# Kernel tuning notes

Hardware: AMD Instinct MI355X
Metric: run time of the kernel (lower is better)

Reference implementation:

```python
import jax, jax.numpy as jnp
import numpy as np

EPS = 1e-15
ATANH_CLIP = 1.0 - 1e-5
C = 1.0  # ball.c = |k|, k = -1.0
SQC = 1.0  # sqrt(C)


def _artanh(x):
    return jnp.arctanh(jnp.clip(x, -ATANH_CLIP, ATANH_CLIP))


def _norm(x):
    return jnp.linalg.norm(x, axis=-1, keepdims=True)


def mobius_add(x, y):
    x2 = jnp.sum(x * x, axis=-1, keepdims=True)
    y2 = jnp.sum(y * y, axis=-1, keepdims=True)
    xy = jnp.sum(x * y, axis=-1, keepdims=True)
    num = (1.0 + 2.0 * C * xy + C * y2) * x + (1.0 - C * x2) * y
    den = 1.0 + 2.0 * C * xy + (C ** 2) * x2 * y2
    return num / jnp.maximum(den, EPS)


def mobius_matvec(M, x):
    # x: [..., d_in], M: [d_out, d_in]
    x_norm = jnp.maximum(_norm(x), EPS)
    mx = x @ M.T
    mx_norm_raw = _norm(mx)
    mx_norm = jnp.maximum(mx_norm_raw, EPS)
    res = jnp.tanh(mx_norm / x_norm * _artanh(SQC * x_norm)) * mx / (mx_norm * SQC)
    return jnp.where(mx_norm_raw <= EPS, 0.0, res)


def mobius_pointwise_mul(w, x):
    x_norm = jnp.maximum(_norm(x), EPS)
    wx = w * x
    wx_norm_raw = _norm(wx)
    wx_norm = jnp.maximum(wx_norm_raw, EPS)
    res = jnp.tanh(wx_norm / x_norm * _artanh(SQC * x_norm)) * wx / (wx_norm * SQC)
    return jnp.where(wx_norm_raw <= EPS, 0.0, res)


def expmap0(u):
    un = jnp.maximum(_norm(u), EPS)
    return jnp.tanh(SQC * un) * u / (SQC * un)


def logmap0(y):
    yn = jnp.maximum(_norm(y), EPS)
    return _artanh(SQC * yn) * y / (SQC * yn)


def one_rnn_transform(W, h, U, x, b):
    Wh = mobius_matvec(W, h)
    Ux = mobius_matvec(U, x)
    return mobius_add(mobius_add(Wh, Ux), b)


def gru_cell(x, hx, weight_ih, weight_hh, bias):
    W_ir, W_ih, W_iz = jnp.split(weight_ih, 3, axis=0)
    W_hr, W_hh, W_hz = jnp.split(weight_hh, 3, axis=0)
    b_r, b_h, b_z = bias[0], bias[1], bias[2]
    z_t = jax.nn.sigmoid(logmap0(one_rnn_transform(W_hz, hx, W_iz, x, b_z)))
    r_t = jax.nn.sigmoid(logmap0(one_rnn_transform(W_hr, hx, W_ir, x, b_r)))
    rh_t = mobius_pointwise_mul(r_t, hx)
    h_tilde = one_rnn_transform(W_hh, rh_t, W_ih, x, b_h)
    delta_h = mobius_add(-hx, h_tilde)
    return mobius_add(hx, mobius_pointwise_mul(z_t, delta_h))


def gru_layer(x_seq, h0, weight_ih, weight_hh, bias):
    def step(hx, xt):
        h = gru_cell(xt, hx, weight_ih, weight_hh, bias)
        return h, h
    h_last, outs = jax.lax.scan(step, h0, x_seq)
    return outs, h_last


def setup_inputs() -> dict:
    key = jax.random.key(0)
    ks = jax.random.split(key, 8)
    T, B, D, H = 256, 64, 512, 512
    stdv = 1.0 / np.sqrt(H)
    inp = {
        # hyperbolic_input=True -> points must lie inside the unit ball; scale small
        "input": jax.random.normal(ks[0], (T, B, D), jnp.float32) * 0.01,
        "h0": jnp.zeros((2, B, H), jnp.float32),
        "weight_ih_1": jax.random.uniform(ks[1], (3 * H, D), jnp.float32, -stdv, stdv),
        "weight_ih_2": jax.random.uniform(ks[2], (3 * H, H), jnp.float32, -stdv, stdv),
        "weight_hh_1": jax.random.uniform(ks[3], (3 * H, H), jnp.float32, -stdv, stdv),
        "weight_hh_2": jax.random.uniform(ks[4], (3 * H, H), jnp.float32, -stdv, stdv),
        # biases initialized as expmap0(randn * 1e-5)
        "bias_1": expmap0(jax.random.normal(ks[5], (3, H), jnp.float32) * 1e-5),
        "bias_2": expmap0(jax.random.normal(ks[6], (3, H), jnp.float32) * 1e-5),
    }
    return inp


def reference(input, h0, weight_ih_1, weight_ih_2, weight_hh_1, weight_hh_2, bias_1, bias_2):
    # hyperbolic_input=True and hyperbolic_hidden_state0=True -> no initial expmap0
    out1, h_last1 = gru_layer(input, h0[0], weight_ih_1, weight_hh_1, bias_1)
    out2, h_last2 = gru_layer(out1, h0[1], weight_ih_2, weight_hh_2, bias_2)
    ht = jnp.stack([h_last1, h_last2])
    return out2, ht
```

## Files before the change

kernel.cpp:

```cpp
#include <hip/hip_runtime.h>
#include <hip/hip_fp16.h>
#include <math.h>
#include <stdint.h>


#define T_  256
#define B_  64
#define H_  512
#define G3_ 1536
#define EPSF 1e-15f
#define CLIPF (1.0f - 1e-5f)
#define SCOPE_AGENT __HIP_MEMORY_SCOPE_AGENT

typedef _Float16 v2h __attribute__((ext_vector_type(2)));

__device__ __forceinline__ float fdot2_(unsigned int w, unsigned int h, float c){
#if __has_builtin(__builtin_amdgcn_fdot2)
  return __builtin_amdgcn_fdot2(__builtin_bit_cast(v2h, w), __builtin_bit_cast(v2h, h), c, false);
#else
  const __half2 wh = __builtin_bit_cast(__half2, w);
  const __half2 hh = __builtin_bit_cast(__half2, h);
  return c + __low2float(wh)*__low2float(hh) + __high2float(wh)*__high2float(hh);
#endif
}

__device__ __forceinline__ float artanh_c(float x){
  x = fminf(fmaxf(x, -CLIPF), CLIPF);
  return 0.5f * logf((1.0f + x) / (1.0f - x));
}
__device__ __forceinline__ float sigmoidf_(float x){ return 1.0f/(1.0f+expf(-x)); }
__device__ __forceinline__ float hsum4(float4 v){ return (v.x+v.y)+(v.z+v.w); }

__device__ __forceinline__ void postf(unsigned long long* p, float x, unsigned tag){
  unsigned long long v = ((unsigned long long)tag << 32) |
                         (unsigned long long)__float_as_uint(x);
  __hip_atomic_store(p, v, __ATOMIC_RELAXED, SCOPE_AGENT);
}
__device__ __forceinline__ float pollf(const unsigned long long* p, unsigned tag){
  unsigned long long v = __hip_atomic_load(p, __ATOMIC_RELAXED, SCOPE_AGENT);
  while ((unsigned)(v >> 32) != tag)
    v = __hip_atomic_load(p, __ATOMIC_RELAXED, SCOPE_AGENT);
  return __uint_as_float((unsigned)v);
}

template<int NS>
__device__ __forceinline__ void wave_reduce_store(float (&v)[NS], float* red, int tid){
  #pragma unroll
  for (int off = 32; off > 0; off >>= 1)
    #pragma unroll
    for (int s = 0; s < NS; s++) v[s] += __shfl_xor(v[s], off);
  if ((tid & 63) == 0)
    #pragma unroll
    for (int s = 0; s < NS; s++) red[s*8 + (tid >> 6)] = v[s];
}

__global__ void k_prep_ih(const float* __restrict__ Wih, float* __restrict__ WihT){
  int i = blockIdx.x * blockDim.x + threadIdx.x;
  if (i >= H_ * G3_) return;
  int k = i / G3_, n = i % G3_;
  WihT[i] = Wih[n * H_ + k];
}

__device__ __forceinline__ uint4 pack8h(const float* s){
  __half2 p0 = __halves2half2(__float2half_rn(s[0]), __float2half_rn(s[1]));
  __half2 p1 = __halves2half2(__float2half_rn(s[2]), __float2half_rn(s[3]));
  __half2 p2 = __halves2half2(__float2half_rn(s[4]), __float2half_rn(s[5]));
  __half2 p3 = __halves2half2(__float2half_rn(s[6]), __float2half_rn(s[7]));
  uint4 r;
  r.x = __builtin_bit_cast(unsigned int, p0);
  r.y = __builtin_bit_cast(unsigned int, p1);
  r.z = __builtin_bit_cast(unsigned int, p2);
  r.w = __builtin_bit_cast(unsigned int, p3);
  return r;
}

__global__ void k_prep_hhR(const float* __restrict__ Whh, uint4* __restrict__ WzrR,
                           uint4* __restrict__ WhcR){
  int i = blockIdx.x * blockDim.x + threadIdx.x;
  if (i < 65536){
    int w = i >> 14, rem = i & 16383;
    int ii = rem >> 9, tid = rem & 511;
    int c = tid & 255, ks = tid >> 8;
    int j = 128*w + (c & 127);
    int row = (c < 128) ? (1024 + j) : j;
    int k0 = ks*256 + ii*8;
    WzrR[i] = pack8h(Whh + row*H_ + k0);
  } else {
    int e = i - 65536;
    int w = e >> 13, rem = e & 8191;
    int q = rem >> 11, rem2 = rem & 2047;
    int ii = rem2 >> 7, c = rem2 & 127;
    int row = 512 + 128*w + c;
    int k0 = q*128 + ii*8;
    WhcR[e] = pack8h(Whh + row*H_ + k0);
  }
}

__global__ __launch_bounds__(256) void k_gemm(const float* __restrict__ A,
                                              const float* __restrict__ Bt,
                                              float* __restrict__ C){
  const int N = G3_, K = H_;
  const int mbase = blockIdx.x * 64, nbase = blockIdx.y * 64;
  __shared__ float As[32][65];
  __shared__ float Bs[32][65];
  const int tid = threadIdx.x;
  const int tm = tid >> 4, tn = tid & 15;
  float acc[4][4] = {};
  for (int k0 = 0; k0 < K; k0 += 32){
    #pragma unroll
    for (int i = 0; i < 8; i++){
      int e = tid + 256*i;
      int m = e >> 5, k = e & 31;
      As[k][m] = A[(size_t)(mbase + m) * K + k0 + k];
      int kk = e >> 6, n = e & 63;
      Bs[kk][n] = Bt[(size_t)(k0 + kk) * N + nbase + n];
    }
    __syncthreads();
    #pragma unroll
    for (int kk = 0; kk < 32; kk++){
      float av[4], bv[4];
      #pragma unroll
      for (int i = 0; i < 4; i++) av[i] = As[kk][tm*4+i];
      #pragma unroll
      for (int j = 0; j < 4; j++) bv[j] = Bs[kk][tn*4+j];
      #pragma unroll
      for (int i = 0; i < 4; i++)
        #pragma unroll
        for (int j = 0; j < 4; j++)
          acc[i][j] = fmaf(av[i], bv[j], acc[i][j]);
    }
    __syncthreads();
  }
  #pragma unroll
  for (int i = 0; i < 4; i++)
    #pragma unroll
    for (int j = 0; j < 4; j++)
      C[(size_t)(mbase + tm*4 + i) * N + nbase + tn*4 + j] = acc[i][j];
}

__global__ void k_nonlin(const float* __restrict__ X, float* __restrict__ D){
  const int row = blockIdx.x;
  const int lane = threadIdx.x;
  const float* x = X + (size_t)row * H_;
  float s = 0.0f;
  for (int k = lane; k < H_; k += 64){ float v = x[k]; s = fmaf(v, v, s); }
  #pragma unroll
  for (int off = 32; off > 0; off >>= 1) s += __shfl_xor(s, off);
  const float xn = fmaxf(sqrtf(s), EPSF);
  const float art = artanh_c(xn);
  float* drow = D + (size_t)row * G3_;
  for (int g = 0; g < 3; g++){
    float* mx = drow + g * H_;
    float s2 = 0.0f;
    for (int k = lane; k < H_; k += 64){ float v = mx[k]; s2 = fmaf(v, v, s2); }
    #pragma unroll
    for (int off = 32; off > 0; off >>= 1) s2 += __shfl_xor(s2, off);
    const float raw = sqrtf(s2);
    const float mn = fmaxf(raw, EPSF);
    const float scale = (raw <= EPSF) ? 0.0f : (tanhf(mn / xn * art) / mn);
    for (int k = lane; k < H_; k += 64) mx[k] *= scale;
  }
}

__global__ __launch_bounds__(512, 2) void k_scan(
    const float* __restrict__ D,
    const uint4* __restrict__ WzrR,
    const uint4* __restrict__ WhcR,
    const float* __restrict__ bias,
    const float* __restrict__ h0,
    float* __restrict__ outbuf,
    float* __restrict__ hlast,
    unsigned long long* __restrict__ hS,
    unsigned long long* __restrict__ wvS,
    unsigned long long* __restrict__ S1s,
    unsigned long long* __restrict__ S3s,
    unsigned long long* __restrict__ S4s)
{
  const int blk = blockIdx.x;
  const int b = blk & 63, w = blk >> 6;
  const int tid = threadIdx.x;
  const int lane = tid & 63, wave = tid >> 6;
  __shared__ __align__(16) __half hh[H_];
  __shared__ __align__(16) float hf[H_];
  __shared__ __align__(16) __half wvh[H_];
  __shared__ __align__(16) float ph[512];
  __shared__ __align__(16) float red[96];
  __shared__ __align__(16) float redW[8];
  __shared__ __align__(16) float xr[16];

  unsigned long long* hRow  = hS  + b*512;
  unsigned long long* wvRow = wvS + b*512;
  unsigned long long* s1Row = S1s + b*64;
  unsigned long long* s3Row = S3s + b*64;
  unsigned long long* s4Row = S4s + b*64;

  const int ks = tid >> 8;
  const int c2 = tid & 127, q = tid >> 7;
  const uint4* wAb = WzrR + (size_t)w*32*512 + tid;
  const uint4* wBb = WhcR + ((size_t)(w*4 + q)*16)*128 + c2;
  uint4 wA[32];
  #pragma unroll
  for (int i = 0; i < 32; i++) wA[i] = wAb[i*512];
  uint4 wB[16];
  #pragma unroll
  for (int i = 0; i < 16; i++) wB[i] = wBb[i*128];

  {
    const float hv0 = h0[b*H_ + tid];
    hf[tid] = hv0;
    hh[tid] = __float2half_rn(hv0);
  }
  const int jg = 128*w + (tid & 127);
  const bool isZ = (tid < 128);
  const bool isGate = (tid < 256);
  const float bval = isGate ? (isZ ? bias[1024 + jg] : bias[jg]) : 0.f;
  const float bcj  = isZ ? bias[512 + jg] : 0.f;
  float B2own, BC2;
  {
    const float vz = bias[1024 + tid], vr = bias[tid], vc = bias[512 + tid];
    float vb[3] = { vz*vz, vr*vr, vc*vc };
    wave_reduce_store<3>(vb, red, tid);
    __syncthreads();
    const float4* p = (const float4*)red;
    const float B2z = hsum4(p[0]) + hsum4(p[1]);
    const float B2r = hsum4(p[2]) + hsum4(p[3]);
    BC2 = hsum4(p[4]) + hsum4(p[5]);
    B2own = isZ ? B2z : B2r;
    __syncthreads();
  }

  const uint4* hh4 = (const uint4*)hh;
  const uint4* wv4 = (const uint4*)wvh;
  const float* Dbase = D + (size_t)b * G3_;

  float zreg = 0.f;
  for (int t = 0; t < T_; t++){
    const unsigned tag = (unsigned)(t + 1);
    const float* U = Dbase + (size_t)t * (B_ * G3_);
    const float yg = isGate ? U[(isZ ? 1024 : 0) + jg] : 0.f;
    const float yc = isZ ? U[512 + jg] : 0.f;

    if (t > 0){
      const float hv = pollf(hRow + tid, (unsigned)t);
      hf[tid] = hv;
      hh[tid] = __float2half_rn(hv);
    }
    __syncthreads();
    const float hv = hf[tid];

    float ap = 0.f;
    #pragma unroll
    for (int i = 0; i < 32; i++){
      const uint4 wr = wA[i];
      const uint4 hp = hh4[ks*32 + i];
      ap = fdot2_(wr.x, hp.x, ap);
      ap = fdot2_(wr.y, hp.y, ap);
      ap = fdot2_(wr.z, hp.z, ap);
      ap = fdot2_(wr.w, hp.w, ap);
    }
    ph[tid] = ap;
    __syncthreads();
    const float a = isGate ? (ph[tid] + ph[tid + 256]) : 0.f;

    {
      float v[11];
      v[0] = hv*hv;
      #pragma unroll
      for (int s = 1; s < 11; s++) v[s] = 0.f;
      if (isGate){
        const int o = isZ ? 1 : 6;
        v[o] = a*a; v[o+1] = a*yg; v[o+2] = yg*yg; v[o+3] = a*bval; v[o+4] = yg*bval;
      }
      wave_reduce_store<11>(v, red, tid);
    }
    __syncthreads();
    float H2;
    { const float4* p = (const float4*)red; H2 = hsum4(p[0]) + hsum4(p[1]); }
    if (wave == 0 && lane < 10){
      float s = 0.f;
      const float* r = red + (1 + lane)*8;
      #pragma unroll
      for (int i = 0; i < 8; i++) s += r[i];
      postf(s1Row + w*16 + lane, s, tag);
    }
    if (wave == 0){
      const int wgi = lane >> 4, s = lane & 15;
      float v = (s < 10) ? pollf(s1Row + wgi*16 + s, tag) : 0.f;
      v += __shfl_xor(v, 16);
      v += __shfl_xor(v, 32);
      if (lane < 16) xr[lane] = v;
    }
    __syncthreads();

    const float xn = fmaxf(sqrtf(H2), EPSF);
    const float art_h = artanh_c(xn);
    if (isGate){
      const int o = isZ ? 0 : 5;
      const float A2 = xr[o], AY = xr[o+1], Yy2 = xr[o+2], AB = xr[o+3], YB = xr[o+4];
      const float mraw = sqrtf(A2);
      const float mnc = fmaxf(mraw, EPSF);
      const float alpha = (mraw <= EPSF) ? 0.f : (tanhf(mnc/xn*art_h)/mnc);
      const float X2 = alpha*alpha*A2, XY = alpha*AY, XB = alpha*AB;
      const float cA1 = 1.f + 2.f*XY + Yy2, cB1 = 1.f - X2;
      const float den1 = fmaxf(1.f + 2.f*XY + X2*Yy2, EPSF), id1 = 1.f/den1;
      const float T2 = fmaxf((cA1*cA1*X2 + 2.f*cA1*cB1*XY + cB1*cB1*Yy2)*id1*id1, 0.f);
      const float TB = (cA1*XB + cB1*YB)*id1;
      const float cA2 = 1.f + 2.f*TB + B2own, cB2 = 1.f - T2;
      const float den2 = fmaxf(1.f + 2.f*TB + T2*B2own, EPSF), id2 = 1.f/den2;
      const float U2 = fmaxf((cA2*cA2*T2 + 2.f*cA2*cB2*TB + cB2*cB2*B2own)*id2*id2, 0.f);
      const float un = fmaxf(sqrtf(U2), EPSF);
      const float lsc = artanh_c(un)/un;
      const float t1el = (cA1*(alpha*a) + cB1*yg)*id1;
      const float uel  = (cA2*t1el + cB2*bval)*id2;
      const float g = sigmoidf_(lsc*uel);
      if (isZ) zreg = g;
      else postf(wvRow + jg, g * hf[jg], tag);
    }
    const float wvv = pollf(wvRow + tid, tag);
    wvh[tid] = __float2half_rn(wvv);
    {
      float v1[1] = { wvv*wvv };
      wave_reduce_store<1>(v1, redW, tid);
    }
    __syncthreads();
    float W2;
    { const float4* p = (const float4*)redW; W2 = hsum4(p[0]) + hsum4(p[1]); }
    const float wraw = sqrtf(W2);
    const float wn = fmaxf(wraw, EPSF);
    const float mu = (wraw <= EPSF) ? 0.f : (tanhf(wn/xn*art_h)/wn);
    const float rhn = fmaxf(mu*wraw, EPSF);

    float cp = 0.f;
    #pragma unroll
    for (int i = 0; i < 16; i++){
      const uint4 wr = wB[i];
      const uint4 rp = wv4[q*16 + i];
      cp = fdot2_(wr.x, rp.x, cp);
      cp = fdot2_(wr.y, rp.y, cp);
      cp = fdot2_(wr.z, rp.z, cp);
      cp = fdot2_(wr.w, rp.w, cp);
    }
    ph[tid] = cp;
    __syncthreads();
    float cel = 0.f, hj = 0.f;
    if (isZ){
      cel = mu * (ph[tid] + ph[tid+128] + ph[tid+256] + ph[tid+384]);
      hj  = hf[jg];
    }
    {
      float v[8] = { cel*cel, cel*yc, yc*yc, cel*bcj, yc*bcj, hj*cel, hj*yc, hj*bcj };
      wave_reduce_store<8>(v, red, tid);
    }
    __syncthreads();
    if (wave == 0 && lane < 8){
      float s = 0.f;
      const float* r = red + lane*8;
      #pragma unroll
      for (int i = 0; i < 8; i++) s += r[i];
      postf(s3Row + w*16 + lane, s, tag);
    }
    if (wave == 0){
      const int wgi = lane >> 4, s = lane & 15;
      float v = (s < 8) ? pollf(s3Row + wgi*16 + s, tag) : 0.f;
      v += __shfl_xor(v, 16);
      v += __shfl_xor(v, 32);
      if (lane < 16) xr[lane] = v;
    }
    __syncthreads();
    const float C2 = xr[0], CY = xr[1], Y2c = xr[2], CB = xr[3],
                YBc = xr[4], HC = xr[5], HYd = xr[6], HBd = xr[7];
    const float craw = sqrtf(C2);
    const float cmn2 = fmaxf(craw, EPSF);
    const float alc = (craw <= EPSF) ? 0.f : (tanhf(cmn2/rhn*artanh_c(rhn))/cmn2);
    const float X2c = alc*alc*C2, XYc = alc*CY, XBc = alc*CB, HXc = alc*HC;
    const float cA1c = 1.f + 2.f*XYc + Y2c, cB1c = 1.f - X2c;
    const float den1c = fmaxf(1.f + 2.f*XYc + X2c*Y2c, EPSF), id1c = 1.f/den1c;
    const float T2c = fmaxf((cA1c*cA1c*X2c + 2.f*cA1c*cB1c*XYc + cB1c*cB1c*Y2c)*id1c*id1c, 0.f);
    const float TBc = (cA1c*XBc + cB1c*YBc)*id1c;
    const float HT1 = (cA1c*HXc + cB1c*HYd)*id1c;
    const float cA2c = 1.f + 2.f*TBc + BC2, cB2c = 1.f - T2c;
    const float den2c = fmaxf(1.f + 2.f*TBc + T2c*BC2, EPSF), id2c = 1.f/den2c;
    const float HTL2 = fmaxf((cA2c*cA2c*T2c + 2.f*cA2c*cB2c*TBc + cB2c*cB2c*BC2)*id2c*id2c, 0.f);
    const float HHTL = (cA2c*HT1 + cB2c*HBd)*id2c;
    const float cAd = 1.f - 2.f*HHTL + HTL2, cBd = 1.f - H2;
    const float dend = fmaxf(1.f - 2.f*HHTL + H2*HTL2, EPSF), idd = 1.f/dend;
    float del = 0.f, w2el = 0.f;
    if (isZ){
      const float t1cel = (cA1c*(alc*cel) + cB1c*yc)*id1c;
      const float htlel = (cA2c*t1cel + cB2c*bcj)*id2c;
      del = (cAd*(-hj) + cBd*htlel)*idd;
      w2el = zreg*del;
    }
    {
      float v[3] = { del*del, w2el*w2el, hj*w2el };
      wave_reduce_store<3>(v, red, tid);
    }
    __syncthreads();
    if (wave == 0 && lane < 3){
      float s = 0.f;
      const float* r = red + lane*8;
      #pragma unroll
      for (int i = 0; i < 8; i++) s += r[i];
      postf(s4Row + w*16 + lane, s, tag);
    }
    if (wave == 0){
      const int wgi = lane >> 4, s = lane & 15;
      float v = (s < 3) ? pollf(s4Row + wgi*16 + s, tag) : 0.f;
      v += __shfl_xor(v, 16);
      v += __shfl_xor(v, 32);
      if (lane < 16) xr[lane] = v;
    }
    __syncthreads();
    const float D2v = xr[0], W22 = xr[1], HW = xr[2];
    const float dnv = fmaxf(sqrtf(D2v), EPSF);
    const float w2raw = sqrtf(W22);
    const float w2n = fmaxf(w2raw, EPSF);
    const float nu = (w2raw <= EPSF) ? 0.f : (tanhf(w2n/dnv*artanh_c(dnv))/w2n);
    const float Y2f = nu*nu*W22, XYf = nu*HW;
    const float cAf = 1.f + 2.f*XYf + Y2f, cBf = 1.f - H2;
    const float denf = fmaxf(1.f + 2.f*XYf + H2*Y2f, EPSF), idf = 1.f/denf;
    if (isZ){
      const float hnew = (cAf*hj + cBf*(nu*w2el))*idf;
      outbuf[(size_t)(t*B_ + b)*H_ + jg] = hnew;
      postf(hRow + jg, hnew, tag);
      if (t == T_-1) hlast[b*H_ + jg] = hnew;
    }
  }
}

extern "C" void kernel_launch(void* const* d_in, const int* in_sizes, int n_in,
                              void* d_out, int out_size, void* d_ws, size_t ws_size,
                              hipStream_t stream){
  (void)in_sizes; (void)n_in; (void)out_size; (void)ws_size;
  const float* input = (const float*)d_in[0];
  const float* h0    = (const float*)d_in[1];
  const float* wih1  = (const float*)d_in[2];
  const float* wih2  = (const float*)d_in[3];
  const float* whh1  = (const float*)d_in[4];
  const float* whh2  = (const float*)d_in[5];
  const float* bias1 = (const float*)d_in[6];
  const float* bias2 = (const float*)d_in[7];
  float* out = (float*)d_out;

  float* A_    = (float*)d_ws;
  float* Dbuf  = A_ + 786432;
  uint4* WzrR  = (uint4*)(Dbuf + 25165824);
  uint4* WhcR  = WzrR + 65536;
  float* comm0 = (float*)(WhcR + 32768);
  unsigned long long* hS1  = (unsigned long long*)comm0;
  unsigned long long* wvS1 = hS1  + 32768;
  unsigned long long* S1a  = wvS1 + 32768;
  unsigned long long* S3a  = S1a  + 4096;
  unsigned long long* S4a  = S3a  + 4096;
  unsigned long long* hS2  = S4a  + 4096;
  unsigned long long* wvS2 = hS2  + 32768;
  unsigned long long* S1b  = wvS2 + 32768;
  unsigned long long* S3b  = S1b  + 4096;
  unsigned long long* S4b  = S3b  + 4096;

  float* out1 = out;
  float* ht   = out + (size_t)T_ * B_ * H_;

  k_prep_ih<<<3072, 256, 0, stream>>>(wih1, A_);
  k_gemm<<<dim3(256, 24), 256, 0, stream>>>(input, A_, Dbuf);
  k_nonlin<<<T_*B_, 64, 0, stream>>>(input, Dbuf);
  k_prep_hhR<<<384, 256, 0, stream>>>(whh1, WzrR, WhcR);
  k_scan<<<256, 512, 0, stream>>>(Dbuf, WzrR, WhcR, bias1, h0, out1, ht,
                                  hS1, wvS1, S1a, S3a, S4a);

  k_prep_ih<<<3072, 256, 0, stream>>>(wih2, A_);
  k_gemm<<<dim3(256, 24), 256, 0, stream>>>(out1, A_, Dbuf);
  k_nonlin<<<T_*B_, 64, 0, stream>>>(out1, Dbuf);
  k_prep_hhR<<<384, 256, 0, stream>>>(whh2, WzrR, WhcR);
  k_scan<<<256, 512, 0, stream>>>(Dbuf, WzrR, WhcR, bias2, h0 + B_*H_, out, ht + B_*H_,
                                  hS2, wvS2, S1b, S3b, S4b);
}
```

Before: 7.808 ms.

## Split recurrent matvec along K across blocks and exchange partial dots

The recurrent scan now has each of the 4 blocks per batch row hold a 128-wide K-slice of all three gate weight matrices for all 512 outputs. Blocks exchange per-element partial dot products through tagged global atomics. Previously blocks split outputs and exchanged hidden state, gate values and several cross-block reduction scalars. With this split every block holds the full hidden state and computes all norms and the gate math redundantly, which removes three global handshake rounds per step, at the cost of more polling traffic and duplicated elementwise work. A tag base separates the two layers because they share the same exchange buffers.

```diff
diff --git a/kernel.cpp b/kernel.cpp
--- a/kernel.cpp
+++ b/kernel.cpp
@@ -30,18 +30,16 @@
 }
 __device__ __forceinline__ float sigmoidf_(float x){ return 1.0f/(1.0f+expf(-x)); }
 __device__ __forceinline__ float hsum4(float4 v){ return (v.x+v.y)+(v.z+v.w); }
+__device__ __forceinline__ float sum8(const float* r){
+  const float4* p = (const float4*)r;
+  return hsum4(p[0]) + hsum4(p[1]);
+}
 
 __device__ __forceinline__ void postf(unsigned long long* p, float x, unsigned tag){
   unsigned long long v = ((unsigned long long)tag << 32) |
                          (unsigned long long)__float_as_uint(x);
   __hip_atomic_store(p, v, __ATOMIC_RELAXED, SCOPE_AGENT);
 }
-__device__ __forceinline__ float pollf(const unsigned long long* p, unsigned tag){
-  unsigned long long v = __hip_atomic_load(p, __ATOMIC_RELAXED, SCOPE_AGENT);
-  while ((unsigned)(v >> 32) != tag)
-    v = __hip_atomic_load(p, __ATOMIC_RELAXED, SCOPE_AGENT);
-  return __uint_as_float((unsigned)v);
-}
 
 template<int NS>
 __device__ __forceinline__ void wave_reduce_store(float (&v)[NS], float* red, int tid){
@@ -52,6 +50,27 @@
   if ((tid & 63) == 0)
     #pragma unroll
     for (int s = 0; s < NS; s++) red[s*8 + (tid >> 6)] = v[s];
+}
+
+__device__ __forceinline__ float gate_val(float a, float y, float bv,
+    float A2, float AY, float Y2, float AB, float YB, float B2,
+    float xn, float art_h){
+  const float mraw = sqrtf(A2);
+  const float mnc = fmaxf(mraw, EPSF);
+  const float alpha = (mraw <= EPSF) ? 0.f : (tanhf(mnc/xn*art_h)/mnc);
+  const float X2 = alpha*alpha*A2, XY = alpha*AY, XB = alpha*AB;
+  const float cA1 = 1.f + 2.f*XY + Y2, cB1 = 1.f - X2;
+  const float den1 = fmaxf(1.f + 2.f*XY + X2*Y2, EPSF), id1 = 1.f/den1;
+  const float T2 = fmaxf((cA1*cA1*X2 + 2.f*cA1*cB1*XY + cB1*cB1*Y2)*id1*id1, 0.f);
+  const float TB = (cA1*XB + cB1*YB)*id1;
+  const float cA2 = 1.f + 2.f*TB + B2, cB2 = 1.f - T2;
+  const float den2 = fmaxf(1.f + 2.f*TB + T2*B2, EPSF), id2 = 1.f/den2;
+  const float U2 = fmaxf((cA2*cA2*T2 + 2.f*cA2*cB2*TB + cB2*cB2*B2)*id2*id2, 0.f);
+  const float un = fmaxf(sqrtf(U2), EPSF);
+  const float lsc = artanh_c(un)/un;
+  const float t1el = (cA1*(alpha*a) + cB1*y)*id1;
+  const float uel  = (cA2*t1el + cB2*bv)*id2;
+  return sigmoidf_(lsc*uel);
 }
 
 __global__ void k_prep_ih(const float* __restrict__ Wih, float* __restrict__ WihT){
@@ -74,26 +93,15 @@
   return r;
 }
 
-__global__ void k_prep_hhR(const float* __restrict__ Whh, uint4* __restrict__ WzrR,
-                           uint4* __restrict__ WhcR){
+__global__ void k_prep_hhR(const float* __restrict__ Whh, uint4* __restrict__ WR){
   int i = blockIdx.x * blockDim.x + threadIdx.x;
-  if (i < 65536){
-    int w = i >> 14, rem = i & 16383;
-    int ii = rem >> 9, tid = rem & 511;
-    int c = tid & 255, ks = tid >> 8;
-    int j = 128*w + (c & 127);
-    int row = (c < 128) ? (1024 + j) : j;
-    int k0 = ks*256 + ii*8;
-    WzrR[i] = pack8h(Whh + row*H_ + k0);
-  } else {
-    int e = i - 65536;
-    int w = e >> 13, rem = e & 8191;
-    int q = rem >> 11, rem2 = rem & 2047;
-    int ii = rem2 >> 7, c = rem2 & 127;
-    int row = 512 + 128*w + c;
-    int k0 = q*128 + ii*8;
-    WhcR[e] = pack8h(Whh + row*H_ + k0);
-  }
+  if (i >= 98304) return;
+  int w = i / 24576, rem = i % 24576;
+  int g = rem / 8192, rem2 = rem % 8192;
+  int ii = rem2 >> 9, tid = rem2 & 511;
+  int row = (g == 0) ? (1024 + tid) : ((g == 1) ? tid : (512 + tid));
+  int k0 = w*128 + ii*8;
+  WR[i] = pack8h(Whh + (size_t)row*H_ + k0);
 }
 
 __global__ __launch_bounds__(256) void k_gemm(const float* __restrict__ A,
@@ -164,167 +172,139 @@
 
 __global__ __launch_bounds__(512, 2) void k_scan(
     const float* __restrict__ D,
-    const uint4* __restrict__ WzrR,
-    const uint4* __restrict__ WhcR,
+    const uint4* __restrict__ WR,
     const float* __restrict__ bias,
     const float* __restrict__ h0,
     float* __restrict__ outbuf,
     float* __restrict__ hlast,
-    unsigned long long* __restrict__ hS,
-    unsigned long long* __restrict__ wvS,
-    unsigned long long* __restrict__ S1s,
-    unsigned long long* __restrict__ S3s,
-    unsigned long long* __restrict__ S4s)
+    unsigned long long* __restrict__ PA,
+    unsigned long long* __restrict__ PB,
+    unsigned tagbase)
 {
   const int blk = blockIdx.x;
   const int b = blk & 63, w = blk >> 6;
   const int tid = threadIdx.x;
-  const int lane = tid & 63, wave = tid >> 6;
   __shared__ __align__(16) __half hh[H_];
-  __shared__ __align__(16) float hf[H_];
   __shared__ __align__(16) __half wvh[H_];
-  __shared__ __align__(16) float ph[512];
-  __shared__ __align__(16) float red[96];
+  __shared__ __align__(16) float red[120];
   __shared__ __align__(16) float redW[8];
-  __shared__ __align__(16) float xr[16];
-
-  unsigned long long* hRow  = hS  + b*512;
-  unsigned long long* wvRow = wvS + b*512;
-  unsigned long long* s1Row = S1s + b*64;
-  unsigned long long* s3Row = S3s + b*64;
-  unsigned long long* s4Row = S4s + b*64;
-
-  const int ks = tid >> 8;
-  const int c2 = tid & 127, q = tid >> 7;
-  const uint4* wAb = WzrR + (size_t)w*32*512 + tid;
-  const uint4* wBb = WhcR + ((size_t)(w*4 + q)*16)*128 + c2;
-  uint4 wA[32];
-  #pragma unroll
-  for (int i = 0; i < 32; i++) wA[i] = wAb[i*512];
-  uint4 wB[16];
-  #pragma unroll
-  for (int i = 0; i < 16; i++) wB[i] = wBb[i*128];
-
+  __shared__ __align__(16) float redS3[32];
+  __shared__ __align__(16) float redS4[24];
+
+  unsigned long long* paRow = PA + (size_t)b*4096;
+  unsigned long long* pbRow = PB + (size_t)b*2048;
+
+  const uint4* wbase = WR + (size_t)w*24576 + tid;
+  uint4 wZ[16], wRr[16], wC[16];
+  #pragma unroll
+  for (int i = 0; i < 16; i++) wZ[i]  = wbase[i*512];
+  #pragma unroll
+  for (int i = 0; i < 16; i++) wRr[i] = wbase[(16+i)*512];
+  #pragma unroll
+  for (int i = 0; i < 16; i++) wC[i]  = wbase[(32+i)*512];
+
+  float h_own = h0[b*H_ + tid];
+  hh[tid] = __float2half_rn(h_own);
+
+  const float bz = bias[1024+tid], br = bias[tid], bc = bias[512+tid];
   {
-    const float hv0 = h0[b*H_ + tid];
-    hf[tid] = hv0;
-    hh[tid] = __float2half_rn(hv0);
+    float vb[3] = { bz*bz, br*br, bc*bc };
+    wave_reduce_store<3>(vb, red, tid);
   }
-  const int jg = 128*w + (tid & 127);
-  const bool isZ = (tid < 128);
-  const bool isGate = (tid < 256);
-  const float bval = isGate ? (isZ ? bias[1024 + jg] : bias[jg]) : 0.f;
-  const float bcj  = isZ ? bias[512 + jg] : 0.f;
-  float B2own, BC2;
-  {
-    const float vz = bias[1024 + tid], vr = bias[tid], vc = bias[512 + tid];
-    float vb[3] = { vz*vz, vr*vr, vc*vc };
-    wave_reduce_store<3>(vb, red, tid);
-    __syncthreads();
-    const float4* p = (const float4*)red;
-    const float B2z = hsum4(p[0]) + hsum4(p[1]);
-    const float B2r = hsum4(p[2]) + hsum4(p[3]);
-    BC2 = hsum4(p[4]) + hsum4(p[5]);
-    B2own = isZ ? B2z : B2r;
-    __syncthreads();
-  }
+  __syncthreads();
+  const float B2z = sum8(red), B2r = sum8(red+8), BC2 = sum8(red+16);
+  __syncthreads();
 
   const uint4* hh4 = (const uint4*)hh;
   const uint4* wv4 = (const uint4*)wvh;
   const float* Dbase = D + (size_t)b * G3_;
 
-  float zreg = 0.f;
+  const int wp1 = (w+1)&3, wp2 = (w+2)&3, wp3 = (w+3)&3;
+  unsigned long long* ownA0 = paRow + (w*2+0)*512 + tid;
+  unsigned long long* ownA1 = paRow + (w*2+1)*512 + tid;
+  unsigned long long* ownB  = pbRow + w*512 + tid;
+  const unsigned long long* qa0 = paRow + (wp1*2+0)*512 + tid;
+  const unsigned long long* qa1 = paRow + (wp1*2+1)*512 + tid;
+  const unsigned long long* qa2 = paRow + (wp2*2+0)*512 + tid;
+  const unsigned long long* qa3 = paRow + (wp2*2+1)*512 + tid;
+  const unsigned long long* qa4 = paRow + (wp3*2+0)*512 + tid;
+  const unsigned long long* qa5 = paRow + (wp3*2+1)*512 + tid;
+  const unsigned long long* qb0 = pbRow + wp1*512 + tid;
+  const unsigned long long* qb1 = pbRow + wp2*512 + tid;
+  const unsigned long long* qb2 = pbRow + wp3*512 + tid;
+
   for (int t = 0; t < T_; t++){
-    const unsigned tag = (unsigned)(t + 1);
+    const unsigned tag = tagbase + (unsigned)t + 1u;
     const float* U = Dbase + (size_t)t * (B_ * G3_);
-    const float yg = isGate ? U[(isZ ? 1024 : 0) + jg] : 0.f;
-    const float yc = isZ ? U[512 + jg] : 0.f;
-
-    if (t > 0){
-      const float hv = pollf(hRow + tid, (unsigned)t);
-      hf[tid] = hv;
-      hh[tid] = __float2half_rn(hv);
-    }
-    __syncthreads();
-    const float hv = hf[tid];
-
-    float ap = 0.f;
-    #pragma unroll
-    for (int i = 0; i < 32; i++){
-      const uint4 wr = wA[i];
-      const uint4 hp = hh4[ks*32 + i];
-      ap = fdot2_(wr.x, hp.x, ap);
-      ap = fdot2_(wr.y, hp.y, ap);
-      ap = fdot2_(wr.z, hp.z, ap);
-      ap = fdot2_(wr.w, hp.w, ap);
-    }
-    ph[tid] = ap;
-    __syncthreads();
-    const float a = isGate ? (ph[tid] + ph[tid + 256]) : 0.f;
-
-    {
-      float v[11];
-      v[0] = hv*hv;
-      #pragma unroll
-      for (int s = 1; s < 11; s++) v[s] = 0.f;
-      if (isGate){
-        const int o = isZ ? 1 : 6;
-        v[o] = a*a; v[o+1] = a*yg; v[o+2] = yg*yg; v[o+3] = a*bval; v[o+4] = yg*bval;
-      }
-      wave_reduce_store<11>(v, red, tid);
-    }
-    __syncthreads();
-    float H2;
-    { const float4* p = (const float4*)red; H2 = hsum4(p[0]) + hsum4(p[1]); }
-    if (wave == 0 && lane < 10){
-      float s = 0.f;
-      const float* r = red + (1 + lane)*8;
-      #pragma unroll
-      for (int i = 0; i < 8; i++) s += r[i];
-      postf(s1Row + w*16 + lane, s, tag);
-    }
-    if (wave == 0){
-      const int wgi = lane >> 4, s = lane & 15;
-      float v = (s < 10) ? pollf(s1Row + wgi*16 + s, tag) : 0.f;
-      v += __shfl_xor(v, 16);
-      v += __shfl_xor(v, 32);
-      if (lane < 16) xr[lane] = v;
-    }
-    __syncthreads();
+    const float yr = U[tid], yc = U[512 + tid], yz = U[1024 + tid];
+
+    float apz = 0.f, apr = 0.f;
+    #pragma unroll
+    for (int i = 0; i < 16; i++){
+      const uint4 hp = hh4[(w<<4) + i];
+      const uint4 z = wZ[i];
+      apz = fdot2_(z.x, hp.x, apz); apz = fdot2_(z.y, hp.y, apz);
+      apz = fdot2_(z.z, hp.z, apz); apz = fdot2_(z.w, hp.w, apz);
+      const uint4 r = wRr[i];
+      apr = fdot2_(r.x, hp.x, apr); apr = fdot2_(r.y, hp.y, apr);
+      apr = fdot2_(r.z, hp.z, apr); apr = fdot2_(r.w, hp.w, apr);
+    }
+    postf(ownA0, apz, tag);
+    postf(ownA1, apr, tag);
+
+    {
+      float v[9] = { h_own*h_own, yz*yz, yz*bz, yr*yr, yr*br,
+                     yc*yc, yc*bc, h_own*yc, h_own*bc };
+      wave_reduce_store<9>(v, red, tid);
+    }
+
+    float az = apz, ar = apr;
+    {
+      float f0=0.f,f1=0.f,f2=0.f,f3=0.f,f4=0.f,f5=0.f;
+      unsigned pend = 0x3fu;
+      do {
+        unsigned long long u;
+        if (pend & 1u ){ u = __hip_atomic_load(qa0, __ATOMIC_RELAXED, SCOPE_AGENT);
+          if ((unsigned)(u>>32)==tag){ f0=__uint_as_float((unsigned)u); pend&=~1u; } }
+        if (pend & 2u ){ u = __hip_atomic_load(qa1, __ATOMIC_RELAXED, SCOPE_AGENT);
+          if ((unsigned)(u>>32)==tag){ f1=__uint_as_float((unsigned)u); pend&=~2u; } }
+        if (pend & 4u ){ u = __hip_atomic_load(qa2, __ATOMIC_RELAXED, SCOPE_AGENT);
+          if ((unsigned)(u>>32)==tag){ f2=__uint_as_float((unsigned)u); pend&=~4u; } }
+        if (pend & 8u ){ u = __hip_atomic_load(qa3, __ATOMIC_RELAXED, SCOPE_AGENT);
+          if ((unsigned)(u>>32)==tag){ f3=__uint_as_float((unsigned)u); pend&=~8u; } }
+        if (pend & 16u){ u = __hip_atomic_load(qa4, __ATOMIC_RELAXED, SCOPE_AGENT);
+          if ((unsigned)(u>>32)==tag){ f4=__uint_as_float((unsigned)u); pend&=~16u; } }
+        if (pend & 32u){ u = __hip_atomic_load(qa5, __ATOMIC_RELAXED, SCOPE_AGENT);
+          if ((unsigned)(u>>32)==tag){ f5=__uint_as_float((unsigned)u); pend&=~32u; } }
+      } while (pend);
+      az += f0 + f2 + f4;
+      ar += f1 + f3 + f5;
+    }
+    {
+      float v[6] = { az*az, az*yz, az*bz, ar*ar, ar*yr, ar*br };
+      wave_reduce_store<6>(v, red + 72, tid);
+    }
+    __syncthreads();
+    const float H2  = sum8(red);
+    const float Y2z = sum8(red+8),  YBz = sum8(red+16);
+    const float Y2r = sum8(red+24), YBr = sum8(red+32);
+    const float Y2c = sum8(red+40), YBc = sum8(red+48);
+    const float HYd = sum8(red+56), HBd = sum8(red+64);
+    const float A2z = sum8(red+72), AYz = sum8(red+80), ABz = sum8(red+88);
+    const float A2r = sum8(red+96), AYr = sum8(red+104), ABr = sum8(red+112);
 
     const float xn = fmaxf(sqrtf(H2), EPSF);
     const float art_h = artanh_c(xn);
-    if (isGate){
-      const int o = isZ ? 0 : 5;
-      const float A2 = xr[o], AY = xr[o+1], Yy2 = xr[o+2], AB = xr[o+3], YB = xr[o+4];
-      const float mraw = sqrtf(A2);
-      const float mnc = fmaxf(mraw, EPSF);
-      const float alpha = (mraw <= EPSF) ? 0.f : (tanhf(mnc/xn*art_h)/mnc);
-      const float X2 = alpha*alpha*A2, XY = alpha*AY, XB = alpha*AB;
-      const float cA1 = 1.f + 2.f*XY + Yy2, cB1 = 1.f - X2;
-      const float den1 = fmaxf(1.f + 2.f*XY + X2*Yy2, EPSF), id1 = 1.f/den1;
-      const float T2 = fmaxf((cA1*cA1*X2 + 2.f*cA1*cB1*XY + cB1*cB1*Yy2)*id1*id1, 0.f);
-      const float TB = (cA1*XB + cB1*YB)*id1;
-      const float cA2 = 1.f + 2.f*TB + B2own, cB2 = 1.f - T2;
-      const float den2 = fmaxf(1.f + 2.f*TB + T2*B2own, EPSF), id2 = 1.f/den2;
-      const float U2 = fmaxf((cA2*cA2*T2 + 2.f*cA2*cB2*TB + cB2*cB2*B2own)*id2*id2, 0.f);
-      const float un = fmaxf(sqrtf(U2), EPSF);
-      const float lsc = artanh_c(un)/un;
-      const float t1el = (cA1*(alpha*a) + cB1*yg)*id1;
-      const float uel  = (cA2*t1el + cB2*bval)*id2;
-      const float g = sigmoidf_(lsc*uel);
-      if (isZ) zreg = g;
-      else postf(wvRow + jg, g * hf[jg], tag);
-    }
-    const float wvv = pollf(wvRow + tid, tag);
+    const float zreg = gate_val(az, yz, bz, A2z, AYz, Y2z, ABz, YBz, B2z, xn, art_h);
+    const float gr   = gate_val(ar, yr, br, A2r, AYr, Y2r, ABr, YBr, B2r, xn, art_h);
+    const float wvv = gr * h_own;
     wvh[tid] = __float2half_rn(wvv);
     {
       float v1[1] = { wvv*wvv };
       wave_reduce_store<1>(v1, redW, tid);
     }
     __syncthreads();
-    float W2;
-    { const float4* p = (const float4*)redW; W2 = hsum4(p[0]) + hsum4(p[1]); }
+    const float W2 = sum8(redW);
     const float wraw = sqrtf(W2);
     const float wn = fmaxf(wraw, EPSF);
     const float mu = (wraw <= EPSF) ? 0.f : (tanhf(wn/xn*art_h)/wn);
@@ -333,42 +313,36 @@
     float cp = 0.f;
     #pragma unroll
     for (int i = 0; i < 16; i++){
-      const uint4 wr = wB[i];
-      const uint4 rp = wv4[q*16 + i];
-      cp = fdot2_(wr.x, rp.x, cp);
-      cp = fdot2_(wr.y, rp.y, cp);
-      cp = fdot2_(wr.z, rp.z, cp);
-      cp = fdot2_(wr.w, rp.w, cp);
-    }
-    ph[tid] = cp;
-    __syncthreads();
-    float cel = 0.f, hj = 0.f;
-    if (isZ){
-      cel = mu * (ph[tid] + ph[tid+128] + ph[tid+256] + ph[tid+384]);
-      hj  = hf[jg];
-    }
-    {
-      float v[8] = { cel*cel, cel*yc, yc*yc, cel*bcj, yc*bcj, hj*cel, hj*yc, hj*bcj };
-      wave_reduce_store<8>(v, red, tid);
-    }
-    __syncthreads();
-    if (wave == 0 && lane < 8){
-      float s = 0.f;
-      const float* r = red + lane*8;
-      #pragma unroll
-      for (int i = 0; i < 8; i++) s += r[i];
-      postf(s3Row + w*16 + lane, s, tag);
-    }
-    if (wave == 0){
-      const int wgi = lane >> 4, s = lane & 15;
-      float v = (s < 8) ? pollf(s3Row + wgi*16 + s, tag) : 0.f;
-      v += __shfl_xor(v, 16);
-      v += __shfl_xor(v, 32);
-      if (lane < 16) xr[lane] = v;
-    }
-    __syncthreads();
-    const float C2 = xr[0], CY = xr[1], Y2c = xr[2], CB = xr[3],
-                YBc = xr[4], HC = xr[5], HYd = xr[6], HBd = xr[7];
+      const uint4 rp = wv4[(w<<4) + i];
+      const uint4 c = wC[i];
+      cp = fdot2_(c.x, rp.x, cp); cp = fdot2_(c.y, rp.y, cp);
+      cp = fdot2_(c.z, rp.z, cp); cp = fdot2_(c.w, rp.w, cp);
+    }
+    postf(ownB, cp, tag);
+    float cdot = cp;
+    {
+      float g0=0.f,g1=0.f,g2=0.f;
+      unsigned pend = 7u;
+      do {
+        unsigned long long u;
+        if (pend & 1u){ u = __hip_atomic_load(qb0, __ATOMIC_RELAXED, SCOPE_AGENT);
+          if ((unsigned)(u>>32)==tag){ g0=__uint_as_float((unsigned)u); pend&=~1u; } }
+        if (pend & 2u){ u = __hip_atomic_load(qb1, __ATOMIC_RELAXED, SCOPE_AGENT);
+          if ((unsigned)(u>>32)==tag){ g1=__uint_as_float((unsigned)u); pend&=~2u; } }
+        if (pend & 4u){ u = __hip_atomic_load(qb2, __ATOMIC_RELAXED, SCOPE_AGENT);
+          if ((unsigned)(u>>32)==tag){ g2=__uint_as_float((unsigned)u); pend&=~4u; } }
+      } while (pend);
+      cdot += g0 + g1 + g2;
+    }
+    const float cel = mu * cdot;
+    const float hj = h_own;
+    {
+      float v[4] = { cel*cel, cel*yc, cel*bc, hj*cel };
+      wave_reduce_store<4>(v, redS3, tid);
+    }
+    __syncthreads();
+    const float C2 = sum8(redS3), CY = sum8(redS3+8),
+                CB = sum8(redS3+16), HC = sum8(redS3+24);
     const float craw = sqrtf(C2);
     const float cmn2 = fmaxf(craw, EPSF);
     const float alc = (craw <= EPSF) ? 0.f : (tanhf(cmn2/rhn*artanh_c(rhn))/cmn2);
@@ -384,34 +358,16 @@
     const float HHTL = (cA2c*HT1 + cB2c*HBd)*id2c;
     const float cAd = 1.f - 2.f*HHTL + HTL2, cBd = 1.f - H2;
     const float dend = fmaxf(1.f - 2.f*HHTL + H2*HTL2, EPSF), idd = 1.f/dend;
-    float del = 0.f, w2el = 0.f;
-    if (isZ){
-      const float t1cel = (cA1c*(alc*cel) + cB1c*yc)*id1c;
-      const float htlel = (cA2c*t1cel + cB2c*bcj)*id2c;
-      del = (cAd*(-hj) + cBd*htlel)*idd;
-      w2el = zreg*del;
-    }
+    const float t1cel = (cA1c*(alc*cel) + cB1c*yc)*id1c;
+    const float htlel = (cA2c*t1cel + cB2c*bc)*id2c;
+    const float del = (cAd*(-hj) + cBd*htlel)*idd;
+    const float w2el = zreg*del;
     {
       float v[3] = { del*del, w2el*w2el, hj*w2el };
-      wave_reduce_store<3>(v, red, tid);
-    }
-    __syncthreads();
-    if (wave == 0 && lane < 3){
-      float s = 0.f;
-      const float* r = red + lane*8;
-      #pragma unroll
-      for (int i = 0; i < 8; i++) s += r[i];
-      postf(s4Row + w*16 + lane, s, tag);
-    }
-    if (wave == 0){
-      const int wgi = lane >> 4, s = lane & 15;
-      float v = (s < 3) ? pollf(s4Row + wgi*16 + s, tag) : 0.f;
-      v += __shfl_xor(v, 16);
-      v += __shfl_xor(v, 32);
-      if (lane < 16) xr[lane] = v;
-    }
-    __syncthreads();
-    const float D2v = xr[0], W22 = xr[1], HW = xr[2];
+      wave_reduce_store<3>(v, redS4, tid);
+    }
+    __syncthreads();
+    const float D2v = sum8(redS4), W22 = sum8(redS4+8), HW = sum8(redS4+16);
     const float dnv = fmaxf(sqrtf(D2v), EPSF);
     const float w2raw = sqrtf(W22);
     const float w2n = fmaxf(w2raw, EPSF);
@@ -419,12 +375,14 @@
     const float Y2f = nu*nu*W22, XYf = nu*HW;
     const float cAf = 1.f + 2.f*XYf + Y2f, cBf = 1.f - H2;
     const float denf = fmaxf(1.f + 2.f*XYf + H2*Y2f, EPSF), idf = 1.f/denf;
-    if (isZ){
-      const float hnew = (cAf*hj + cBf*(nu*w2el))*idf;
-      outbuf[(size_t)(t*B_ + b)*H_ + jg] = hnew;
-      postf(hRow + jg, hnew, tag);
-      if (t == T_-1) hlast[b*H_ + jg] = hnew;
-    }
+    const float hnew = (cAf*hj + cBf*(nu*w2el))*idf;
+    h_own = hnew;
+    hh[tid] = __float2half_rn(hnew);
+    if (w == 0){
+      outbuf[(size_t)(t*B_ + b)*H_ + tid] = hnew;
+      if (t == T_-1) hlast[b*H_ + tid] = hnew;
+    }
+    __syncthreads();
   }
 }
 
@@ -444,19 +402,9 @@
 
   float* A_    = (float*)d_ws;
   float* Dbuf  = A_ + 786432;
-  uint4* WzrR  = (uint4*)(Dbuf + 25165824);
-  uint4* WhcR  = WzrR + 65536;
-  float* comm0 = (float*)(WhcR + 32768);
-  unsigned long long* hS1  = (unsigned long long*)comm0;
-  unsigned long long* wvS1 = hS1  + 32768;
-  unsigned long long* S1a  = wvS1 + 32768;
-  unsigned long long* S3a  = S1a  + 4096;
-  unsigned long long* S4a  = S3a  + 4096;
-  unsigned long long* hS2  = S4a  + 4096;
-  unsigned long long* wvS2 = hS2  + 32768;
-  unsigned long long* S1b  = wvS2 + 32768;
-  unsigned long long* S3b  = S1b  + 4096;
-  unsigned long long* S4b  = S3b  + 4096;
+  uint4* WR    = (uint4*)(Dbuf + 25165824);
+  unsigned long long* PA = (unsigned long long*)(WR + 98304);
+  unsigned long long* PB = PA + 262144;
 
   float* out1 = out;
   float* ht   = out + (size_t)T_ * B_ * H_;
@@ -464,14 +412,12 @@
   k_prep_ih<<<3072, 256, 0, stream>>>(wih1, A_);
   k_gemm<<<dim3(256, 24), 256, 0, stream>>>(input, A_, Dbuf);
   k_nonlin<<<T_*B_, 64, 0, stream>>>(input, Dbuf);
-  k_prep_hhR<<<384, 256, 0, stream>>>(whh1, WzrR, WhcR);
-  k_scan<<<256, 512, 0, stream>>>(Dbuf, WzrR, WhcR, bias1, h0, out1, ht,
-                                  hS1, wvS1, S1a, S3a, S4a);
+  k_prep_hhR<<<384, 256, 0, stream>>>(whh1, WR);
+  k_scan<<<256, 512, 0, stream>>>(Dbuf, WR, bias1, h0, out1, ht, PA, PB, 0u);
 
   k_prep_ih<<<3072, 256, 0, stream>>>(wih2, A_);
   k_gemm<<<dim3(256, 24), 256, 0, stream>>>(out1, A_, Dbuf);
   k_nonlin<<<T_*B_, 64, 0, stream>>>(out1, Dbuf);
-  k_prep_hhR<<<384, 256, 0, stream>>>(whh2, WzrR, WhcR);
-  k_scan<<<256, 512, 0, stream>>>(Dbuf, WzrR, WhcR, bias2, h0 + B_*H_, out, ht + B_*H_,
-                                  hS2, wvS2, S1b, S3b, S4b);
-}
+  k_prep_hhR<<<384, 256, 0, stream>>>(whh2, WR);
+  k_scan<<<256, 512, 0, stream>>>(Dbuf, WR, bias2, h0 + B_*H_, out, ht + B_*H_, PA, PB, 256u);
+}
```

After: 11.08 ms. +41.9%, slower.
